# Kernel tuning notes

Hardware: AMD Instinct MI355X
Metric: run time of the kernel (lower is better)

## Reference

```python
import jax, jax.numpy as jnp
import numpy as np
import math

B, SQ, SK, D = 16, 2048, 2048, 64


def setup_inputs() -> dict:
    key = jax.random.key(0)
    kq, kk, kv, kl = jax.random.split(key, 4)
    queries = jax.random.normal(kq, (B, SQ, D), dtype=jnp.float32)
    keys = jax.random.normal(kk, (B, SK, D), dtype=jnp.float32)
    values = jax.random.normal(kv, (B, SK, D), dtype=jnp.float32)
    # valid key lengths in [1, SK]
    valid_lens = jax.random.randint(kl, (B,), 1, SK + 1, dtype=jnp.int32)
    return {"queries": queries, "keys": keys, "values": values, "valid_lens": valid_lens}


def reference(queries, keys, values, valid_lens):
    d = queries.shape[-1]
    # [B, SQ, SK] raw scores
    scores = jnp.einsum("bqd,bkd->bqk", queries, keys) / math.sqrt(d)
    # masked_softmax: key positions >= valid_len are set to -1e6 (d2l semantics)
    kpos = jnp.arange(scores.shape[-1], dtype=jnp.int32)  # [SK]
    mask = kpos[None, None, :] < valid_lens[:, None, None]  # [B,1,SK] -> broadcast
    scores = jnp.where(mask, scores, jnp.float32(-1e6))
    attn = jax.nn.softmax(scores, axis=-1)
    # dropout rate is 0.0 -> identity
    return jnp.einsum("bqk,bkd->bqd", attn, values)
```

## Files before the change

kernel.cpp:

```cpp
#include <hip/hip_runtime.h>

#define NB 16
#define SQL 2048
#define SKL 2048
#define DH 64
#define NSPLIT 4
#define CHUNK 512

typedef __attribute__((ext_vector_type(8))) short bf16x8;
typedef __attribute__((ext_vector_type(4))) unsigned short u16x4;
typedef __attribute__((ext_vector_type(8))) unsigned short u16x8;
typedef __attribute__((ext_vector_type(4))) float f32x4;

#define LOG2E 1.4426950408889634f
#define K1 (0.125f * LOG2E)

__device__ __forceinline__ unsigned short f2bf(float f) {
    unsigned int u = __builtin_bit_cast(unsigned int, f);
    u += 0x7fffu + ((u >> 16) & 1u);
    return (unsigned short)(u >> 16);
}

__global__ __launch_bounds__(256) void prep_kernel(
    const float* __restrict__ Q, const float* __restrict__ K,
    const float* __restrict__ V,
    unsigned short* __restrict__ Qb, unsigned short* __restrict__ Kb,
    unsigned short* __restrict__ Vt) {
    const int blk = blockIdx.x;
    if (blk < 2048) {
        const float* src = (blk < 1024) ? Q : K;
        unsigned short* dst = (blk < 1024) ? Qb : Kb;
        const size_t base = ((size_t)(blk & 1023) * 256 + threadIdx.x) * 8;
        float4 a = *(const float4*)(src + base);
        float4 b = *(const float4*)(src + base + 4);
        u16x8 o;
        o[0] = f2bf(a.x); o[1] = f2bf(a.y); o[2] = f2bf(a.z); o[3] = f2bf(a.w);
        o[4] = f2bf(b.x); o[5] = f2bf(b.y); o[6] = f2bf(b.z); o[7] = f2bf(b.w);
        *(u16x8*)(dst + base) = o;
    } else {
        const int t  = blk - 2048;
        const int b  = t >> 5;
        const int kb = (t & 31) << 6;
        __shared__ float tile[64][65];
        const int tid = threadIdx.x;
        {
            const int r  = tid >> 2;
            const int cg = (tid & 3) << 4;
            const float* vsrc = V + ((size_t)b * SKL + (kb + r)) * DH;
            #pragma unroll
            for (int i = 0; i < 4; ++i) {
                float4 x = *(const float4*)(vsrc + cg + i * 4);
                tile[r][cg + i*4 + 0] = x.x;
                tile[r][cg + i*4 + 1] = x.y;
                tile[r][cg + i*4 + 2] = x.z;
                tile[r][cg + i*4 + 3] = x.w;
            }
        }
        __syncthreads();
        {
            const int d  = tid >> 2;
            const int kg = (tid & 3) << 4;
            unsigned short* dst = Vt + ((size_t)b * DH + d) * SKL + kb + kg;
            u16x8 o0, o1;
            #pragma unroll
            for (int j = 0; j < 8; ++j) o0[j] = f2bf(tile[kg + j][d]);
            #pragma unroll
            for (int j = 0; j < 8; ++j) o1[j] = f2bf(tile[kg + 8 + j][d]);
            *(u16x8*)(dst)     = o0;
            *(u16x8*)(dst + 8) = o1;
        }
    }
}

__global__ __launch_bounds__(256, 4) void attn_kernel(
    const unsigned short* __restrict__ Qb,
    const unsigned short* __restrict__ Kb,
    const unsigned short* __restrict__ Vt,
    const int* __restrict__ valid_lens,
    float* __restrict__ Opart,
    float2* __restrict__ MLpart) {
    const int qblk  = blockIdx.x;
    const int split = blockIdx.y;
    const int b     = blockIdx.z;

    const int valid  = valid_lens[b];
    const int kstart = split * CHUNK;
    if (kstart >= valid) return;
    const int kend   = (valid < kstart + CHUNK) ? valid : (kstart + CHUNK);
    const int ntiles = (kend - kstart + 63) >> 6;

    const int tid  = threadIdx.x;
    const int wave = tid >> 6;
    const int lane = tid & 63;
    const int c16  = lane & 15;
    const int quad = lane >> 4;
    const int h    = c16 & 7;

    __shared__ unsigned short Klds[64][64];
    __shared__ unsigned short Vlds[64][64];
    __shared__ unsigned short Plds[4][16][64];

    const int q0 = qblk * 64 + wave * 16;
    const unsigned short* qptr = Qb + ((size_t)b * SQL + q0 + c16) * DH;
    const bf16x8 qf0 = *(const bf16x8*)(qptr + quad * 8);
    const bf16x8 qf1 = *(const bf16x8*)(qptr + 32 + quad * 8);

    const unsigned short* kbase = Kb + (size_t)b * SKL * DH;
    const unsigned short* vbase = Vt + (size_t)b * DH * SKL;

    const f32x4 zero = {0.f, 0.f, 0.f, 0.f};
    f32x4 o[4];
    #pragma unroll
    for (int i = 0; i < 4; ++i) o[i] = zero;
    float mrow = -1e30f, lrow = 0.f;

    u16x8 kreg[2], vreg[2];
    {
        #pragma unroll
        for (int i = 0; i < 2; ++i) {
            const int c = i * 256 + tid, r = c >> 3, col = (c & 7) << 3;
            kreg[i] = *(const u16x8*)(kbase + (size_t)(kstart + r) * DH + col);
            vreg[i] = *(const u16x8*)(vbase + (size_t)r * SKL + kstart + col);
        }
    }

    for (int kt = 0; kt < ntiles; ++kt) {
        const int kb = kstart + (kt << 6);
        __syncthreads();
        #pragma unroll
        for (int i = 0; i < 2; ++i) {
            const int c = i * 256 + tid, r = c >> 3;
            const int pc = ((c & 7) ^ (r & 7)) << 3;
            *(u16x8*)&Klds[r][pc] = kreg[i];
            *(u16x8*)&Vlds[r][pc] = vreg[i];
        }
        __syncthreads();
        if (kt + 1 < ntiles) {
            const int kn = kb + 64;
            #pragma unroll
            for (int i = 0; i < 2; ++i) {
                const int c = i * 256 + tid, r = c >> 3, col = (c & 7) << 3;
                kreg[i] = *(const u16x8*)(kbase + (size_t)(kn + r) * DH + col);
                vreg[i] = *(const u16x8*)(vbase + (size_t)r * SKL + kn + col);
            }
        }

        f32x4 s[4];
        #pragma unroll
        for (int t = 0; t < 4; ++t) {
            s[t] = zero;
            const bf16x8 kf0 = *(const bf16x8*)&Klds[t*16 + c16][(quad       ^ h) << 3];
            const bf16x8 kf1 = *(const bf16x8*)&Klds[t*16 + c16][((quad + 4) ^ h) << 3];
            s[t] = __builtin_amdgcn_mfma_f32_16x16x32_bf16(kf0, qf0, s[t], 0, 0, 0);
            s[t] = __builtin_amdgcn_mfma_f32_16x16x32_bf16(kf1, qf1, s[t], 0, 0, 0);
        }

        if (kb + 64 > kend) {
            #pragma unroll
            for (int t = 0; t < 4; ++t)
                #pragma unroll
                for (int r = 0; r < 4; ++r)
                    if (kb + t * 16 + quad * 4 + r >= kend) s[t][r] = -1e30f;
        }

        float tmax = -1e30f;
        #pragma unroll
        for (int t = 0; t < 4; ++t)
            #pragma unroll
            for (int r = 0; r < 4; ++r) tmax = fmaxf(tmax, s[t][r]);
        tmax = fmaxf(tmax, __shfl_xor(tmax, 16));
        tmax = fmaxf(tmax, __shfl_xor(tmax, 32));

        const float mnew  = fmaxf(mrow, 0.125f * tmax);
        const float alpha = exp2f((mrow - mnew) * LOG2E);
        const float mk    = mnew * LOG2E;
        float rs = 0.f;
        #pragma unroll
        for (int t = 0; t < 4; ++t)
            #pragma unroll
            for (int r = 0; r < 4; ++r) {
                const float p = exp2f(fmaf(s[t][r], K1, -mk));
                s[t][r] = p;
                rs += p;
            }
        rs += __shfl_xor(rs, 16);
        rs += __shfl_xor(rs, 32);
        lrow = lrow * alpha + rs;
        mrow = mnew;
        #pragma unroll
        for (int i = 0; i < 4; ++i) o[i] *= alpha;

        #pragma unroll
        for (int t = 0; t < 4; ++t) {
            u16x4 pw;
            pw[0] = f2bf(s[t][0]); pw[1] = f2bf(s[t][1]);
            pw[2] = f2bf(s[t][2]); pw[3] = f2bf(s[t][3]);
            const int ch = 2 * t + (quad >> 1);
            *(u16x4*)&Plds[wave][c16][((ch ^ h) << 3) + ((quad & 1) << 2)] = pw;
        }
        const bf16x8 pf0 = *(const bf16x8*)&Plds[wave][c16][(quad       ^ h) << 3];
        const bf16x8 pf1 = *(const bf16x8*)&Plds[wave][c16][((quad + 4) ^ h) << 3];

        #pragma unroll
        for (int dt = 0; dt < 4; ++dt) {
            const bf16x8 vf0 = *(const bf16x8*)&Vlds[dt*16 + c16][(quad       ^ h) << 3];
            const bf16x8 vf1 = *(const bf16x8*)&Vlds[dt*16 + c16][((quad + 4) ^ h) << 3];
            o[dt] = __builtin_amdgcn_mfma_f32_16x16x32_bf16(vf0, pf0, o[dt], 0, 0, 0);
            o[dt] = __builtin_amdgcn_mfma_f32_16x16x32_bf16(vf1, pf1, o[dt], 0, 0, 0);
        }
    }

    float* op = Opart + (((size_t)b * NSPLIT + split) * SQL + q0 + c16) * DH + quad * 4;
    #pragma unroll
    for (int dt = 0; dt < 4; ++dt) *(f32x4*)(op + dt * 16) = o[dt];
    if (quad == 0)
        MLpart[((size_t)b * NSPLIT + split) * SQL + q0 + c16] = make_float2(mrow, lrow);
}

__global__ __launch_bounds__(256) void reduce_kernel(
    const float* __restrict__ Opart, const float2* __restrict__ MLpart,
    const int* __restrict__ valid_lens, float* __restrict__ out) {
    const int b   = blockIdx.y;
    const int tid = threadIdx.x;
    const int q   = blockIdx.x * 64 + (tid >> 2);
    const int dg  = (tid & 3) << 4;
    const int ns  = (valid_lens[b] + CHUNK - 1) / CHUNK;

    float m[NSPLIT], l[NSPLIT];
    float M = -1e30f;
    for (int s = 0; s < ns; ++s) {
        float2 ml = MLpart[((size_t)b * NSPLIT + s) * SQL + q];
        m[s] = ml.x; l[s] = ml.y;
        M = fmaxf(M, ml.x);
    }
    float L = 0.f;
    f32x4 acc[4];
    #pragma unroll
    for (int i = 0; i < 4; ++i) acc[i] = (f32x4){0.f, 0.f, 0.f, 0.f};
    for (int s = 0; s < ns; ++s) {
        const float w = exp2f((m[s] - M) * LOG2E);
        L += l[s] * w;
        const float* p = Opart + (((size_t)b * NSPLIT + s) * SQL + q) * DH + dg;
        #pragma unroll
        for (int i = 0; i < 4; ++i) acc[i] += w * *(const f32x4*)(p + i * 4);
    }
    const float inv = 1.0f / L;
    float* op = out + ((size_t)b * SQL + q) * DH + dg;
    #pragma unroll
    for (int i = 0; i < 4; ++i) *(f32x4*)(op + i * 4) = acc[i] * inv;
}

extern "C" void kernel_launch(void* const* d_in, const int* in_sizes, int n_in,
                              void* d_out, int out_size, void* d_ws, size_t ws_size,
                              hipStream_t stream) {
    const float* Q  = (const float*)d_in[0];
    const float* K  = (const float*)d_in[1];
    const float* V  = (const float*)d_in[2];
    const int*   vl = (const int*)d_in[3];
    float* out = (float*)d_out;

    unsigned short* Qb = (unsigned short*)d_ws;
    unsigned short* Kb = Qb + (size_t)NB * SQL * DH;
    unsigned short* Vt = Kb + (size_t)NB * SKL * DH;
    float*  Opart  = (float*)(Vt + (size_t)NB * SKL * DH);
    float2* MLpart = (float2*)(Opart + (size_t)NB * NSPLIT * SQL * DH);

    prep_kernel<<<dim3(2560), dim3(256), 0, stream>>>(Q, K, V, Qb, Kb, Vt);
    attn_kernel<<<dim3(SQL / 64, NSPLIT, NB), dim3(256), 0, stream>>>(
        Qb, Kb, Vt, vl, Opart, MLpart);
    reduce_kernel<<<dim3(SQL / 64, NB), dim3(256), 0, stream>>>(
        Opart, MLpart, vl, out);
}
```

Measured before the change: 111.0 us.

## Switch attention to 32x32x16 MFMA tiles, finer KV split, bf16 partial outputs

Moves the attention kernel from 16x16x32 to 32x32x16 bf16 MFMA. Each wave now handles 32 query rows and each block 128, which increases K/V reuse per LDS load and removes one shuffle stage in the row reductions. The KV split doubles to 8 chunks of 256 keys to keep enough blocks in flight. Partial outputs are stored as bf16 instead of fp32 to halve the partial-buffer traffic into the reduce kernel, at some cost in accuracy. Register pressure rises, so the occupancy hint drops from 4 to 3 blocks.

```diff
diff --git a/kernel.cpp b/kernel.cpp
--- a/kernel.cpp
+++ b/kernel.cpp
@@ -4,13 +4,14 @@
 #define SQL 2048
 #define SKL 2048
 #define DH 64
-#define NSPLIT 4
-#define CHUNK 512
-
-typedef __attribute__((ext_vector_type(8))) short bf16x8;
-typedef __attribute__((ext_vector_type(4))) unsigned short u16x4;
-typedef __attribute__((ext_vector_type(8))) unsigned short u16x8;
-typedef __attribute__((ext_vector_type(4))) float f32x4;
+#define NSPLIT 8
+#define CHUNK 256
+
+typedef __attribute__((ext_vector_type(8)))  short bf16x8;
+typedef __attribute__((ext_vector_type(4)))  unsigned short u16x4;
+typedef __attribute__((ext_vector_type(8)))  unsigned short u16x8;
+typedef __attribute__((ext_vector_type(4)))  float f32x4;
+typedef __attribute__((ext_vector_type(16))) float f32x16;
 
 #define LOG2E 1.4426950408889634f
 #define K1 (0.125f * LOG2E)
@@ -19,6 +20,9 @@
     unsigned int u = __builtin_bit_cast(unsigned int, f);
     u += 0x7fffu + ((u >> 16) & 1u);
     return (unsigned short)(u >> 16);
+}
+__device__ __forceinline__ float bf2f(unsigned short h) {
+    return __builtin_bit_cast(float, (unsigned int)h << 16);
 }
 
 __global__ __launch_bounds__(256) void prep_kernel(
@@ -72,12 +76,12 @@
     }
 }
 
-__global__ __launch_bounds__(256, 4) void attn_kernel(
+__global__ __launch_bounds__(256, 3) void attn_kernel(
     const unsigned short* __restrict__ Qb,
     const unsigned short* __restrict__ Kb,
     const unsigned short* __restrict__ Vt,
     const int* __restrict__ valid_lens,
-    float* __restrict__ Opart,
+    unsigned short* __restrict__ Opart,
     float2* __restrict__ MLpart) {
     const int qblk  = blockIdx.x;
     const int split = blockIdx.y;
@@ -92,36 +96,36 @@
     const int tid  = threadIdx.x;
     const int wave = tid >> 6;
     const int lane = tid & 63;
-    const int c16  = lane & 15;
-    const int quad = lane >> 4;
-    const int h    = c16 & 7;
+    const int l31  = lane & 31;
+    const int h2   = lane >> 5;
+    const int sw   = l31 & 7;
 
     __shared__ unsigned short Klds[64][64];
     __shared__ unsigned short Vlds[64][64];
-    __shared__ unsigned short Plds[4][16][64];
-
-    const int q0 = qblk * 64 + wave * 16;
-    const unsigned short* qptr = Qb + ((size_t)b * SQL + q0 + c16) * DH;
-    const bf16x8 qf0 = *(const bf16x8*)(qptr + quad * 8);
-    const bf16x8 qf1 = *(const bf16x8*)(qptr + 32 + quad * 8);
+    __shared__ unsigned short Plds[4][32][64];
+
+    const int q0 = qblk * 128 + wave * 32;
+    const unsigned short* qptr = Qb + ((size_t)b * SQL + q0 + l31) * DH + h2 * 8;
+    bf16x8 qf[4];
+    #pragma unroll
+    for (int ks = 0; ks < 4; ++ks) qf[ks] = *(const bf16x8*)(qptr + ks * 16);
 
     const unsigned short* kbase = Kb + (size_t)b * SKL * DH;
     const unsigned short* vbase = Vt + (size_t)b * DH * SKL;
 
-    const f32x4 zero = {0.f, 0.f, 0.f, 0.f};
-    f32x4 o[4];
-    #pragma unroll
-    for (int i = 0; i < 4; ++i) o[i] = zero;
+    f32x16 o[2];
+    #pragma unroll
+    for (int i = 0; i < 2; ++i)
+        #pragma unroll
+        for (int r = 0; r < 16; ++r) o[i][r] = 0.f;
     float mrow = -1e30f, lrow = 0.f;
 
     u16x8 kreg[2], vreg[2];
-    {
-        #pragma unroll
-        for (int i = 0; i < 2; ++i) {
-            const int c = i * 256 + tid, r = c >> 3, col = (c & 7) << 3;
-            kreg[i] = *(const u16x8*)(kbase + (size_t)(kstart + r) * DH + col);
-            vreg[i] = *(const u16x8*)(vbase + (size_t)r * SKL + kstart + col);
-        }
+    #pragma unroll
+    for (int i = 0; i < 2; ++i) {
+        const int c = i * 256 + tid, r = c >> 3, col = (c & 7) << 3;
+        kreg[i] = *(const u16x8*)(kbase + (size_t)(kstart + r) * DH + col);
+        vreg[i] = *(const u16x8*)(vbase + (size_t)r * SKL + kstart + col);
     }
 
     for (int kt = 0; kt < ntiles; ++kt) {
@@ -145,30 +149,33 @@
             }
         }
 
-        f32x4 s[4];
-        #pragma unroll
-        for (int t = 0; t < 4; ++t) {
-            s[t] = zero;
-            const bf16x8 kf0 = *(const bf16x8*)&Klds[t*16 + c16][(quad       ^ h) << 3];
-            const bf16x8 kf1 = *(const bf16x8*)&Klds[t*16 + c16][((quad + 4) ^ h) << 3];
-            s[t] = __builtin_amdgcn_mfma_f32_16x16x32_bf16(kf0, qf0, s[t], 0, 0, 0);
-            s[t] = __builtin_amdgcn_mfma_f32_16x16x32_bf16(kf1, qf1, s[t], 0, 0, 0);
+        f32x16 s[2];
+        #pragma unroll
+        for (int t = 0; t < 2; ++t) {
+            #pragma unroll
+            for (int r = 0; r < 16; ++r) s[t][r] = 0.f;
+            #pragma unroll
+            for (int ks = 0; ks < 4; ++ks) {
+                const bf16x8 kf = *(const bf16x8*)
+                    &Klds[t * 32 + l31][((2 * ks + h2) ^ sw) << 3];
+                s[t] = __builtin_amdgcn_mfma_f32_32x32x16_bf16(kf, qf[ks], s[t], 0, 0, 0);
+            }
         }
 
         if (kb + 64 > kend) {
             #pragma unroll
-            for (int t = 0; t < 4; ++t)
+            for (int t = 0; t < 2; ++t)
                 #pragma unroll
-                for (int r = 0; r < 4; ++r)
-                    if (kb + t * 16 + quad * 4 + r >= kend) s[t][r] = -1e30f;
+                for (int r = 0; r < 16; ++r)
+                    if (kb + t * 32 + (r & 3) + 8 * (r >> 2) + 4 * h2 >= kend)
+                        s[t][r] = -1e30f;
         }
 
         float tmax = -1e30f;
         #pragma unroll
-        for (int t = 0; t < 4; ++t)
-            #pragma unroll
-            for (int r = 0; r < 4; ++r) tmax = fmaxf(tmax, s[t][r]);
-        tmax = fmaxf(tmax, __shfl_xor(tmax, 16));
+        for (int t = 0; t < 2; ++t)
+            #pragma unroll
+            for (int r = 0; r < 16; ++r) tmax = fmaxf(tmax, s[t][r]);
         tmax = fmaxf(tmax, __shfl_xor(tmax, 32));
 
         const float mnew  = fmaxf(mrow, 0.125f * tmax);
@@ -176,49 +183,64 @@
         const float mk    = mnew * LOG2E;
         float rs = 0.f;
         #pragma unroll
-        for (int t = 0; t < 4; ++t)
-            #pragma unroll
-            for (int r = 0; r < 4; ++r) {
+        for (int t = 0; t < 2; ++t)
+            #pragma unroll
+            for (int r = 0; r < 16; ++r) {
                 const float p = exp2f(fmaf(s[t][r], K1, -mk));
                 s[t][r] = p;
                 rs += p;
             }
-        rs += __shfl_xor(rs, 16);
         rs += __shfl_xor(rs, 32);
         lrow = lrow * alpha + rs;
         mrow = mnew;
         #pragma unroll
-        for (int i = 0; i < 4; ++i) o[i] *= alpha;
-
-        #pragma unroll
-        for (int t = 0; t < 4; ++t) {
-            u16x4 pw;
-            pw[0] = f2bf(s[t][0]); pw[1] = f2bf(s[t][1]);
-            pw[2] = f2bf(s[t][2]); pw[3] = f2bf(s[t][3]);
-            const int ch = 2 * t + (quad >> 1);
-            *(u16x4*)&Plds[wave][c16][((ch ^ h) << 3) + ((quad & 1) << 2)] = pw;
-        }
-        const bf16x8 pf0 = *(const bf16x8*)&Plds[wave][c16][(quad       ^ h) << 3];
-        const bf16x8 pf1 = *(const bf16x8*)&Plds[wave][c16][((quad + 4) ^ h) << 3];
-
-        #pragma unroll
-        for (int dt = 0; dt < 4; ++dt) {
-            const bf16x8 vf0 = *(const bf16x8*)&Vlds[dt*16 + c16][(quad       ^ h) << 3];
-            const bf16x8 vf1 = *(const bf16x8*)&Vlds[dt*16 + c16][((quad + 4) ^ h) << 3];
-            o[dt] = __builtin_amdgcn_mfma_f32_16x16x32_bf16(vf0, pf0, o[dt], 0, 0, 0);
-            o[dt] = __builtin_amdgcn_mfma_f32_16x16x32_bf16(vf1, pf1, o[dt], 0, 0, 0);
-        }
-    }
-
-    float* op = Opart + (((size_t)b * NSPLIT + split) * SQL + q0 + c16) * DH + quad * 4;
-    #pragma unroll
-    for (int dt = 0; dt < 4; ++dt) *(f32x4*)(op + dt * 16) = o[dt];
-    if (quad == 0)
-        MLpart[((size_t)b * NSPLIT + split) * SQL + q0 + c16] = make_float2(mrow, lrow);
+        for (int i = 0; i < 2; ++i)
+            #pragma unroll
+            for (int r = 0; r < 16; ++r) o[i][r] *= alpha;
+
+        #pragma unroll
+        for (int t = 0; t < 2; ++t)
+            #pragma unroll
+            for (int g = 0; g < 4; ++g) {
+                u16x4 pw;
+                pw[0] = f2bf(s[t][g * 4 + 0]); pw[1] = f2bf(s[t][g * 4 + 1]);
+                pw[2] = f2bf(s[t][g * 4 + 2]); pw[3] = f2bf(s[t][g * 4 + 3]);
+                const int unit = (4 * t + g) ^ sw;
+                *(u16x4*)&Plds[wave][l31][(unit << 3) + (h2 << 2)] = pw;
+            }
+        bf16x8 pf[4];
+        #pragma unroll
+        for (int ks = 0; ks < 4; ++ks)
+            pf[ks] = *(const bf16x8*)&Plds[wave][l31][((2 * ks + h2) ^ sw) << 3];
+
+        #pragma unroll
+        for (int dt = 0; dt < 2; ++dt)
+            #pragma unroll
+            for (int ks = 0; ks < 4; ++ks) {
+                const bf16x8 vf = *(const bf16x8*)
+                    &Vlds[dt * 32 + l31][((2 * ks + h2) ^ sw) << 3];
+                o[dt] = __builtin_amdgcn_mfma_f32_32x32x16_bf16(vf, pf[ks], o[dt], 0, 0, 0);
+            }
+    }
+
+    unsigned short* op = Opart +
+        (((size_t)b * NSPLIT + split) * SQL + q0 + l31) * DH;
+    #pragma unroll
+    for (int dt = 0; dt < 2; ++dt)
+        #pragma unroll
+        for (int g = 0; g < 4; ++g) {
+            u16x4 ow;
+            ow[0] = f2bf(o[dt][g * 4 + 0]); ow[1] = f2bf(o[dt][g * 4 + 1]);
+            ow[2] = f2bf(o[dt][g * 4 + 2]); ow[3] = f2bf(o[dt][g * 4 + 3]);
+            *(u16x4*)(op + dt * 32 + 8 * g + 4 * h2) = ow;
+        }
+    if (h2 == 0)
+        MLpart[((size_t)b * NSPLIT + split) * SQL + q0 + l31] =
+            make_float2(mrow, lrow);
 }
 
 __global__ __launch_bounds__(256) void reduce_kernel(
-    const float* __restrict__ Opart, const float2* __restrict__ MLpart,
+    const unsigned short* __restrict__ Opart, const float2* __restrict__ MLpart,
     const int* __restrict__ valid_lens, float* __restrict__ out) {
     const int b   = blockIdx.y;
     const int tid = threadIdx.x;
@@ -234,20 +256,30 @@
         M = fmaxf(M, ml.x);
     }
     float L = 0.f;
-    f32x4 acc[4];
-    #pragma unroll
-    for (int i = 0; i < 4; ++i) acc[i] = (f32x4){0.f, 0.f, 0.f, 0.f};
+    float acc[16];
+    #pragma unroll
+    for (int i = 0; i < 16; ++i) acc[i] = 0.f;
     for (int s = 0; s < ns; ++s) {
         const float w = exp2f((m[s] - M) * LOG2E);
         L += l[s] * w;
-        const float* p = Opart + (((size_t)b * NSPLIT + s) * SQL + q) * DH + dg;
-        #pragma unroll
-        for (int i = 0; i < 4; ++i) acc[i] += w * *(const f32x4*)(p + i * 4);
+        const unsigned short* p =
+            Opart + (((size_t)b * NSPLIT + s) * SQL + q) * DH + dg;
+        u16x8 a0 = *(const u16x8*)(p);
+        u16x8 a1 = *(const u16x8*)(p + 8);
+        #pragma unroll
+        for (int i = 0; i < 8; ++i) acc[i]     += w * bf2f(a0[i]);
+        #pragma unroll
+        for (int i = 0; i < 8; ++i) acc[8 + i] += w * bf2f(a1[i]);
     }
     const float inv = 1.0f / L;
     float* op = out + ((size_t)b * SQL + q) * DH + dg;
-    #pragma unroll
-    for (int i = 0; i < 4; ++i) *(f32x4*)(op + i * 4) = acc[i] * inv;
+    f32x4 ov;
+    #pragma unroll
+    for (int i = 0; i < 4; ++i) {
+        ov[0] = acc[i*4+0] * inv; ov[1] = acc[i*4+1] * inv;
+        ov[2] = acc[i*4+2] * inv; ov[3] = acc[i*4+3] * inv;
+        *(f32x4*)(op + i * 4) = ov;
+    }
 }
 
 extern "C" void kernel_launch(void* const* d_in, const int* in_sizes, int n_in,
@@ -262,11 +294,11 @@
     unsigned short* Qb = (unsigned short*)d_ws;
     unsigned short* Kb = Qb + (size_t)NB * SQL * DH;
     unsigned short* Vt = Kb + (size_t)NB * SKL * DH;
-    float*  Opart  = (float*)(Vt + (size_t)NB * SKL * DH);
+    unsigned short* Opart = Vt + (size_t)NB * SKL * DH;
     float2* MLpart = (float2*)(Opart + (size_t)NB * NSPLIT * SQL * DH);
 
     prep_kernel<<<dim3(2560), dim3(256), 0, stream>>>(Q, K, V, Qb, Kb, Vt);
-    attn_kernel<<<dim3(SQL / 64, NSPLIT, NB), dim3(256), 0, stream>>>(
+    attn_kernel<<<dim3(SQL / 128, NSPLIT, NB), dim3(256), 0, stream>>>(
         Qb, Kb, Vt, vl, Opart, MLpart);
     reduce_kernel<<<dim3(SQL / 64, NB), dim3(256), 0, stream>>>(
         Opart, MLpart, vl, out);
```

Result: no change. 110.8 us (-0.2%).
